# Performance work log

Measured on AMD Instinct MI355X. Metric: run time of the kernel, lower is better.

The kernel has to match this reference:

```python
import jax, jax.numpy as jnp
import numpy as np

B, IN, H = 1024, 2048, 2048
W_BIT = A_BIT = I_BIT = R_BIT = 8


def fake_quant(x, bits):
    # brevitas CommonQuant: signed, narrow-range, const scale 1.0 ->
    # int scale s = 1/(2^(b-1)-1); q = clip(round(x/s), -n, n); dq = q*s.
    n = 2.0 ** (bits - 1) - 1.0
    q = jnp.clip(x * n, -n, n)
    q = q + jax.lax.stop_gradient(jnp.round(q) - q)  # STE round
    return q / n


def setup_inputs() -> dict:
    key = jax.random.key(0)
    ks = jax.random.split(key, 7)
    std = 1.0 / np.sqrt(H)  # reset_parameters: uniform(-std, std)
    return {
        "x": jax.random.normal(ks[0], (B, IN), jnp.float32),
        "hx": jax.random.normal(ks[1], (B, H), jnp.float32),
        "cx": jax.random.normal(ks[2], (B, H), jnp.float32),
        "w_x2h": jax.random.uniform(ks[3], (4 * H, IN), jnp.float32, -std, std),
        "b_x2h": jax.random.uniform(ks[4], (4 * H,), jnp.float32, -std, std),
        "w_h2h": jax.random.uniform(ks[5], (4 * H, H), jnp.float32, -std, std),
        "b_h2h": jax.random.uniform(ks[6], (4 * H,), jnp.float32, -std, std),
    }


def reference(x, hx, cx, w_x2h, b_x2h, w_h2h, b_h2h):
    x_q = fake_quant(x, I_BIT)                      # input_quant
    wx_q = fake_quant(w_x2h, W_BIT)                 # CommonWeightQuant
    wh_q = fake_quant(w_h2h, W_BIT)
    gates = (jnp.einsum('bi,gi->bg', x_q, wx_q) + b_x2h
             + jnp.einsum('bh,gh->bg', hx, wh_q) + b_h2h)  # [B, 4H]
    f, i, g, o = jnp.split(gates, 4, axis=1)        # forget, input, cell, out
    f = fake_quant(jax.nn.sigmoid(f), A_BIT)
    i = fake_quant(jax.nn.sigmoid(i), A_BIT)
    g = fake_quant(jnp.tanh(g), A_BIT)
    o = fake_quant(jax.nn.sigmoid(o), A_BIT)
    c_new = f * cx + i * g
    h_new = o * fake_quant(jnp.tanh(c_new), A_BIT)
    c_out = fake_quant(c_new, R_BIT)                # recurrent_quant
    return (h_new, c_out)
```

## Files before the change

kernel.cpp:

```cpp
#include <hip/hip_runtime.h>
#include <stdint.h>
#include <math.h>

typedef __attribute__((ext_vector_type(4))) int i32x4;
typedef __attribute__((ext_vector_type(4))) float f32x4;

#define GLD16(gp, lp)                                                     \
  __builtin_amdgcn_global_load_lds(                                       \
      (__attribute__((address_space(1))) void*)(gp),                      \
      (__attribute__((address_space(3))) void*)(lp), 16, 0, 0)

__global__ void __launch_bounds__(256) k_prep_w(const float* __restrict__ wx,
                                                const float* __restrict__ wh,
                                                signed char* __restrict__ Wq) {
  int i = blockIdx.x * 256 + threadIdx.x;
  int e = i << 2;
  int g = e >> 12;
  int c = e & 4095;
  const float* src = (c < 2048) ? (wx + g * 2048 + c) : (wh + g * 2048 + (c - 2048));
  float4 v = *(const float4*)src;
  char4 o;
  o.x = (signed char)(int)rint(fmin(fmax((double)v.x * 127.0, -127.0), 127.0));
  o.y = (signed char)(int)rint(fmin(fmax((double)v.y * 127.0, -127.0), 127.0));
  o.z = (signed char)(int)rint(fmin(fmax((double)v.z * 127.0, -127.0), 127.0));
  o.w = (signed char)(int)rint(fmin(fmax((double)v.w * 127.0, -127.0), 127.0));
  *(char4*)(Wq + e) = o;
}

__global__ void __launch_bounds__(256) k_prep_a(const float* __restrict__ x,
                                                const float* __restrict__ hx,
                                                signed char* __restrict__ Aq) {
  int i = blockIdx.x * 256 + threadIdx.x;
  int e = i << 2;
  int b = e >> 11;
  int c = e & 2047;
  float4 xv = *(const float4*)(x + b * 2048 + c);
  float4 hv = *(const float4*)(hx + b * 2048 + c);
  float xa[4] = {xv.x, xv.y, xv.z, xv.w};
  float ha[4] = {hv.x, hv.y, hv.z, hv.w};
  char4 q4, s1, s2, s3, s4, s5;
  signed char* qp = (signed char*)&q4;
  signed char* p1 = (signed char*)&s1;
  signed char* p2 = (signed char*)&s2;
  signed char* p3 = (signed char*)&s3;
  signed char* p4 = (signed char*)&s4;
  signed char* p5 = (signed char*)&s5;
  #pragma unroll
  for (int j = 0; j < 4; ++j) {
    qp[j] = (signed char)(int)rint(fmin(fmax((double)xa[j] * 127.0, -127.0), 127.0));
    double r = (double)ha[j];
    double d1 = rint(r * 16.0);     r -= d1 * 0x1p-4;
    double d2 = rint(r * 0x1p11);   r -= d2 * 0x1p-11;
    double d3 = rint(r * 0x1p18);   r -= d3 * 0x1p-18;
    double d4 = rint(r * 0x1p25);   r -= d4 * 0x1p-25;
    double d5 = rint(r * 0x1p32);
    p1[j] = (signed char)(int)d1;
    p2[j] = (signed char)(int)d2;
    p3[j] = (signed char)(int)d3;
    p4[j] = (signed char)(int)d4;
    p5[j] = (signed char)(int)d5;
  }
  size_t base = (size_t)b * 12288;
  *(char4*)(Aq + base + 0 * 2048 + c) = s5;
  *(char4*)(Aq + base + 1 * 2048 + c) = s4;
  *(char4*)(Aq + base + 2 * 2048 + c) = s3;
  *(char4*)(Aq + base + 3 * 2048 + c) = s2;
  *(char4*)(Aq + base + 4 * 2048 + c) = s1;
  *(char4*)(Aq + base + 5 * 2048 + c) = q4;
}

__global__ void __launch_bounds__(256, 3) k_gemm_lstm(
    const signed char* __restrict__ Aq, const signed char* __restrict__ Wq,
    const float* __restrict__ bx, const float* __restrict__ bh,
    const float* __restrict__ cx, float* __restrict__ out) {
  __shared__ __align__(16) signed char smem[24576];
  signed char* As = smem;
  signed char* Bs = smem + 16384;

  const int t  = threadIdx.x;
  const int wv = t >> 6;
  const int ln = t & 63;
  const int wm = wv & 1;
  const int wn = wv >> 1;
  const int lr = ln & 15;
  const int q  = ln >> 4;

  const int j0 = blockIdx.x * 16;
  const int m0 = blockIdx.y * 128;

  int sA[4];
  #pragma unroll
  for (int is = 0; is < 4; ++is) {
    int s = is * 256 + t;
    int r = s >> 3;
    int c = s & 7;
    int cp = c ^ (r & 7);
    sA[is] = (m0 + r) * 12288 + cp * 16;
  }
  int sB[2];
  #pragma unroll
  for (int is = 0; is < 2; ++is) {
    int s = is * 256 + t;
    int r = s >> 3;
    int c = s & 7;
    int cp = c ^ (r & 7);
    int wrow = (r >> 4) * 2048 + j0 + (r & 15);
    sB[is] = wrow * 4096 + cp * 16;
  }

  int aoff[4], boff[2];
  const int swz = lr & 7;
  #pragma unroll
  for (int mf = 0; mf < 4; ++mf)
    aoff[mf] = (wm * 64 + mf * 16 + lr) * 128 + ((q ^ swz) * 16);
  #pragma unroll
  for (int nf = 0; nf < 2; ++nf)
    boff[nf] = (wn * 32 + nf * 16 + lr) * 128 + ((q ^ swz) * 16);

  i32x4 acc[4][2];
  f32x4 Hh[4][2], Hl[4][2];
  #pragma unroll
  for (int mf = 0; mf < 4; ++mf)
    #pragma unroll
    for (int nf = 0; nf < 2; ++nf)
      acc[mf][nf] = (i32x4){0, 0, 0, 0};

  #pragma unroll 1
  for (int ph = 0; ph < 6; ++ph) {
    const int kA = ph * 2048;
    const int kB = (ph < 5) ? 2048 : 0;
    #pragma unroll 1
    for (int it = 0; it < 16; ++it) {
      const int kk = it * 128;
      __syncthreads();
      #pragma unroll
      for (int is = 0; is < 4; ++is)
        GLD16(Aq + sA[is] + kA + kk, As + is * 4096 + wv * 1024);
      #pragma unroll
      for (int is = 0; is < 2; ++is)
        GLD16(Wq + sB[is] + kB + kk, Bs + is * 4096 + wv * 1024);
      asm volatile("s_waitcnt vmcnt(0)" ::: "memory");
      __syncthreads();
      #pragma unroll
      for (int s = 0; s < 2; ++s) {
        const int sx = s << 6;
        i32x4 af[4], bf[2];
        #pragma unroll
        for (int mf = 0; mf < 4; ++mf) af[mf] = *(const i32x4*)&As[aoff[mf] ^ sx];
        #pragma unroll
        for (int nf = 0; nf < 2; ++nf) bf[nf] = *(const i32x4*)&Bs[boff[nf] ^ sx];
        #pragma unroll
        for (int mf = 0; mf < 4; ++mf)
          #pragma unroll
          for (int nf = 0; nf < 2; ++nf)
            acc[mf][nf] = __builtin_amdgcn_mfma_i32_16x16x64_i8(
                af[mf], bf[nf], acc[mf][nf], 0, 0, 0);
      }
    }
    if (ph == 0) {
      #pragma unroll
      for (int mf = 0; mf < 4; ++mf)
        #pragma unroll
        for (int nf = 0; nf < 2; ++nf) {
          #pragma unroll
          for (int r = 0; r < 4; ++r) {
            Hh[mf][nf][r] = (float)acc[mf][nf][r];
            Hl[mf][nf][r] = 0.f;
          }
          acc[mf][nf] = (i32x4){0, 0, 0, 0};
        }
    } else if (ph < 5) {
      #pragma unroll
      for (int mf = 0; mf < 4; ++mf)
        #pragma unroll
        for (int nf = 0; nf < 2; ++nf) {
          #pragma unroll
          for (int r = 0; r < 4; ++r) {
            float tv = Hh[mf][nf][r] * 0x1p-7f;
            float S  = (float)acc[mf][nf][r];
            float sm = tv + S;
            float z  = sm - tv;
            float e  = (tv - (sm - z)) + (S - z);
            Hl[mf][nf][r] = Hl[mf][nf][r] * 0x1p-7f + e;
            Hh[mf][nf][r] = sm;
          }
          acc[mf][nf] = (i32x4){0, 0, 0, 0};
        }
    }
  }

  const double invsq = 1.0 / 16129.0;
  const double hsc   = 0x1p-4 / 127.0;

  float (*Lgo)[128][17] = (float(*)[128][17])smem;

  __syncthreads();
  if (wn == 1) {
    #pragma unroll
    for (int mf = 0; mf < 4; ++mf) {
      #pragma unroll
      for (int nf = 0; nf < 2; ++nf) {
        int gate = 2 + nf;
        int gcol = gate * 2048 + j0 + lr;
        double bsum = (double)bx[gcol] + (double)bh[gcol];
        #pragma unroll
        for (int r = 0; r < 4; ++r) {
          double Sx = (double)acc[mf][nf][r];
          double Hd = ((double)Hh[mf][nf][r] + (double)Hl[mf][nf][r]) * hsc;
          double pre = Sx * invsq + Hd + bsum;
          double av = (gate == 2) ? tanh(pre) : (1.0 / (1.0 + exp(-pre)));
          double qv = rint(fmin(fmax(av * 127.0, -127.0), 127.0));
          int m = wm * 64 + mf * 16 + q * 4 + r;
          Lgo[nf][m][lr] = (float)qv;
        }
      }
    }
  }
  __syncthreads();
  if (wn == 0) {
    #pragma unroll
    for (int mf = 0; mf < 4; ++mf) {
      int gcf = j0 + lr;
      int gci = 2048 + j0 + lr;
      double bf_ = (double)bx[gcf] + (double)bh[gcf];
      double bi_ = (double)bx[gci] + (double)bh[gci];
      #pragma unroll
      for (int r = 0; r < 4; ++r) {
        int m = wm * 64 + mf * 16 + q * 4 + r;
        double fpre = (double)acc[mf][0][r] * invsq +
                      ((double)Hh[mf][0][r] + (double)Hl[mf][0][r]) * hsc + bf_;
        double ipre = (double)acc[mf][1][r] * invsq +
                      ((double)Hh[mf][1][r] + (double)Hl[mf][1][r]) * hsc + bi_;
        double fs = 1.0 / (1.0 + exp(-fpre));
        double is = 1.0 / (1.0 + exp(-ipre));
        double fv = rint(fmin(fmax(fs * 127.0, -127.0), 127.0)) / 127.0;
        double iv = rint(fmin(fmax(is * 127.0, -127.0), 127.0)) / 127.0;
        double gv = (double)Lgo[0][m][lr] / 127.0;
        double ov = (double)Lgo[1][m][lr] / 127.0;
        int row = m0 + m;
        int col = j0 + lr;
        double cn = fv * (double)cx[row * 2048 + col] + iv * gv;
        double tq = rint(fmin(fmax(tanh(cn) * 127.0, -127.0), 127.0)) / 127.0;
        double hv = ov * tq;
        double cq = rint(fmin(fmax(cn * 127.0, -127.0), 127.0)) / 127.0;
        out[row * 2048 + col] = (float)hv;
        out[2097152 + row * 2048 + col] = (float)cq;
      }
    }
  }
}

extern "C" void kernel_launch(void* const* d_in, const int* in_sizes, int n_in,
                              void* d_out, int out_size, void* d_ws, size_t ws_size,
                              hipStream_t stream) {
  const float* x  = (const float*)d_in[0];
  const float* hx = (const float*)d_in[1];
  const float* cx = (const float*)d_in[2];
  const float* wx = (const float*)d_in[3];
  const float* bx = (const float*)d_in[4];
  const float* wh = (const float*)d_in[5];
  const float* bh = (const float*)d_in[6];
  float* out = (float*)d_out;

  signed char* Wq = (signed char*)d_ws;
  signed char* Aq = (signed char*)d_ws + 33554432;

  k_prep_w<<<dim3(32768), dim3(256), 0, stream>>>(wx, wh, Wq);
  k_prep_a<<<dim3(2048), dim3(256), 0, stream>>>(x, hx, Aq);
  k_gemm_lstm<<<dim3(128, 8), dim3(256), 0, stream>>>(Aq, Wq, bx, bh, cx, out);
}
```

Measured before the change: 389.3 us.

## Double-buffer LDS tiles to overlap global loads with MFMA compute

Flattens the phase/iteration loops into a single 96-step loop and uses two LDS buffers so the next K-tile is fetched with global_load_lds while the current tile feeds the int8 MFMAs. This drops one barrier per iteration and hides global-load latency behind compute. It doubles shared memory per block, which could limit occupancy.

```diff
diff --git a/kernel.cpp b/kernel.cpp
--- a/kernel.cpp
+++ b/kernel.cpp
@@ -73,9 +73,7 @@
     const signed char* __restrict__ Aq, const signed char* __restrict__ Wq,
     const float* __restrict__ bx, const float* __restrict__ bh,
     const float* __restrict__ cx, float* __restrict__ out) {
-  __shared__ __align__(16) signed char smem[24576];
-  signed char* As = smem;
-  signed char* Bs = smem + 16384;
+  __shared__ __align__(16) signed char smem[49152];
 
   const int t  = threadIdx.x;
   const int wv = t >> 6;
@@ -125,68 +123,90 @@
     for (int nf = 0; nf < 2; ++nf)
       acc[mf][nf] = (i32x4){0, 0, 0, 0};
 
+  {
+    #pragma unroll
+    for (int is = 0; is < 4; ++is)
+      GLD16(Aq + sA[is], smem + is * 4096 + wv * 1024);
+    #pragma unroll
+    for (int is = 0; is < 2; ++is)
+      GLD16(Wq + sB[is] + 2048, smem + 16384 + is * 4096 + wv * 1024);
+  }
+  asm volatile("s_waitcnt vmcnt(0)" ::: "memory");
+  __syncthreads();
+
+  int lbase = 0;
   #pragma unroll 1
-  for (int ph = 0; ph < 6; ++ph) {
-    const int kA = ph * 2048;
-    const int kB = (ph < 5) ? 2048 : 0;
-    #pragma unroll 1
-    for (int it = 0; it < 16; ++it) {
-      const int kk = it * 128;
-      __syncthreads();
+  for (int g = 0; g < 96; ++g) {
+    if (g < 95) {
+      const int gn  = g + 1;
+      const int phn = gn >> 4;
+      const int kkn = (gn & 15) << 7;
+      const int kAn = phn * 2048 + kkn;
+      const int kBn = ((phn < 5) ? 2048 : 0) + kkn;
+      const int nb  = lbase ^ 24576;
       #pragma unroll
       for (int is = 0; is < 4; ++is)
-        GLD16(Aq + sA[is] + kA + kk, As + is * 4096 + wv * 1024);
+        GLD16(Aq + sA[is] + kAn, smem + nb + is * 4096 + wv * 1024);
       #pragma unroll
       for (int is = 0; is < 2; ++is)
-        GLD16(Wq + sB[is] + kB + kk, Bs + is * 4096 + wv * 1024);
-      asm volatile("s_waitcnt vmcnt(0)" ::: "memory");
-      __syncthreads();
-      #pragma unroll
-      for (int s = 0; s < 2; ++s) {
-        const int sx = s << 6;
-        i32x4 af[4], bf[2];
-        #pragma unroll
-        for (int mf = 0; mf < 4; ++mf) af[mf] = *(const i32x4*)&As[aoff[mf] ^ sx];
-        #pragma unroll
-        for (int nf = 0; nf < 2; ++nf) bf[nf] = *(const i32x4*)&Bs[boff[nf] ^ sx];
+        GLD16(Wq + sB[is] + kBn, smem + nb + 16384 + is * 4096 + wv * 1024);
+    }
+
+    const signed char* As = smem + lbase;
+    const signed char* Bs = smem + lbase + 16384;
+    #pragma unroll
+    for (int s = 0; s < 2; ++s) {
+      const int sx = s << 6;
+      i32x4 af[4], bf[2];
+      #pragma unroll
+      for (int mf = 0; mf < 4; ++mf) af[mf] = *(const i32x4*)&As[aoff[mf] ^ sx];
+      #pragma unroll
+      for (int nf = 0; nf < 2; ++nf) bf[nf] = *(const i32x4*)&Bs[boff[nf] ^ sx];
+      #pragma unroll
+      for (int mf = 0; mf < 4; ++mf)
+        #pragma unroll
+        for (int nf = 0; nf < 2; ++nf)
+          acc[mf][nf] = __builtin_amdgcn_mfma_i32_16x16x64_i8(
+              af[mf], bf[nf], acc[mf][nf], 0, 0, 0);
+    }
+
+    if ((g & 15) == 15) {
+      const int ph = g >> 4;
+      if (ph == 0) {
         #pragma unroll
         for (int mf = 0; mf < 4; ++mf)
           #pragma unroll
-          for (int nf = 0; nf < 2; ++nf)
-            acc[mf][nf] = __builtin_amdgcn_mfma_i32_16x16x64_i8(
-                af[mf], bf[nf], acc[mf][nf], 0, 0, 0);
+          for (int nf = 0; nf < 2; ++nf) {
+            #pragma unroll
+            for (int r = 0; r < 4; ++r) {
+              Hh[mf][nf][r] = (float)acc[mf][nf][r];
+              Hl[mf][nf][r] = 0.f;
+            }
+            acc[mf][nf] = (i32x4){0, 0, 0, 0};
+          }
+      } else if (ph < 5) {
+        #pragma unroll
+        for (int mf = 0; mf < 4; ++mf)
+          #pragma unroll
+          for (int nf = 0; nf < 2; ++nf) {
+            #pragma unroll
+            for (int r = 0; r < 4; ++r) {
+              float tv = Hh[mf][nf][r] * 0x1p-7f;
+              float S  = (float)acc[mf][nf][r];
+              float sm = tv + S;
+              float z  = sm - tv;
+              float e  = (tv - (sm - z)) + (S - z);
+              Hl[mf][nf][r] = Hl[mf][nf][r] * 0x1p-7f + e;
+              Hh[mf][nf][r] = sm;
+            }
+            acc[mf][nf] = (i32x4){0, 0, 0, 0};
+          }
       }
     }
-    if (ph == 0) {
-      #pragma unroll
-      for (int mf = 0; mf < 4; ++mf)
-        #pragma unroll
-        for (int nf = 0; nf < 2; ++nf) {
-          #pragma unroll
-          for (int r = 0; r < 4; ++r) {
-            Hh[mf][nf][r] = (float)acc[mf][nf][r];
-            Hl[mf][nf][r] = 0.f;
-          }
-          acc[mf][nf] = (i32x4){0, 0, 0, 0};
-        }
-    } else if (ph < 5) {
-      #pragma unroll
-      for (int mf = 0; mf < 4; ++mf)
-        #pragma unroll
-        for (int nf = 0; nf < 2; ++nf) {
-          #pragma unroll
-          for (int r = 0; r < 4; ++r) {
-            float tv = Hh[mf][nf][r] * 0x1p-7f;
-            float S  = (float)acc[mf][nf][r];
-            float sm = tv + S;
-            float z  = sm - tv;
-            float e  = (tv - (sm - z)) + (S - z);
-            Hl[mf][nf][r] = Hl[mf][nf][r] * 0x1p-7f + e;
-            Hh[mf][nf][r] = sm;
-          }
-          acc[mf][nf] = (i32x4){0, 0, 0, 0};
-        }
-    }
+
+    asm volatile("s_waitcnt vmcnt(0)" ::: "memory");
+    __syncthreads();
+    lbase ^= 24576;
   }
 
   const double invsq = 1.0 / 16129.0;
@@ -194,7 +214,6 @@
 
   float (*Lgo)[128][17] = (float(*)[128][17])smem;
 
-  __syncthreads();
   if (wn == 1) {
     #pragma unroll
     for (int mf = 0; mf < 4; ++mf) {
```

Measured after the change: 360.8 us. 7.3% less time.

## Triple-buffer A tiles in LDS and stream W fragments directly into registers

Applied to the files above, without the earlier changes.

The K loop becomes one flat software-pipelined loop of 96 steps. A tiles are prefetched two steps ahead into three rotating LDS buffers using async global-to-LDS loads. W fragments skip LDS and are loaded straight into double-buffered registers one step ahead. Each step uses a single barrier with a partial vmcnt wait, and the per-phase accumulator folding moves into the loop body. The aim is to hide global-load latency behind the MFMA work and drop the double sync per iteration. In exchange, LDS use doubles to 48 KB and register pressure rises, which could limit occupancy under the 3-block launch bound.

```diff
diff --git a/kernel.cpp b/kernel.cpp
--- a/kernel.cpp
+++ b/kernel.cpp
@@ -73,9 +73,7 @@
     const signed char* __restrict__ Aq, const signed char* __restrict__ Wq,
     const float* __restrict__ bx, const float* __restrict__ bh,
     const float* __restrict__ cx, float* __restrict__ out) {
-  __shared__ __align__(16) signed char smem[24576];
-  signed char* As = smem;
-  signed char* Bs = smem + 16384;
+  __shared__ __align__(16) signed char smem[49152];
 
   const int t  = threadIdx.x;
   const int wv = t >> 6;
@@ -97,25 +95,17 @@
     int cp = c ^ (r & 7);
     sA[is] = (m0 + r) * 12288 + cp * 16;
   }
-  int sB[2];
-  #pragma unroll
-  for (int is = 0; is < 2; ++is) {
-    int s = is * 256 + t;
-    int r = s >> 3;
-    int c = s & 7;
-    int cp = c ^ (r & 7);
-    int wrow = (r >> 4) * 2048 + j0 + (r & 15);
-    sB[is] = wrow * 4096 + cp * 16;
-  }
-
-  int aoff[4], boff[2];
+
+  int aoff[4];
   const int swz = lr & 7;
   #pragma unroll
   for (int mf = 0; mf < 4; ++mf)
     aoff[mf] = (wm * 64 + mf * 16 + lr) * 128 + ((q ^ swz) * 16);
+
+  const signed char* pB[2];
   #pragma unroll
   for (int nf = 0; nf < 2; ++nf)
-    boff[nf] = (wn * 32 + nf * 16 + lr) * 128 + ((q ^ swz) * 16);
+    pB[nf] = Wq + (size_t)((wn * 2 + nf) * 2048 + j0 + lr) * 4096 + q * 16;
 
   i32x4 acc[4][2];
   f32x4 Hh[4][2], Hl[4][2];
@@ -125,69 +115,116 @@
     for (int nf = 0; nf < 2; ++nf)
       acc[mf][nf] = (i32x4){0, 0, 0, 0};
 
+  i32x4 B0[2][2], B1[2][2];
+
+  {
+    #pragma unroll
+    for (int is = 0; is < 4; ++is)
+      GLD16(Aq + sA[is], smem + is * 4096 + wv * 1024);
+    #pragma unroll
+    for (int is = 0; is < 4; ++is)
+      GLD16(Aq + sA[is] + 128, smem + 16384 + is * 4096 + wv * 1024);
+    #pragma unroll
+    for (int nf = 0; nf < 2; ++nf)
+      #pragma unroll
+      for (int s = 0; s < 2; ++s)
+        B0[nf][s] = *(const i32x4*)(pB[nf] + 2048 + s * 64);
+  }
+  asm volatile("s_waitcnt vmcnt(0)" ::: "memory");
+  __builtin_amdgcn_s_barrier();
+  __builtin_amdgcn_sched_barrier(0);
+
+  int cur = 0;
+  int stg = 32768;
+
+#define FOLD(G)                                                            \
+  if (((G) & 15) == 15) {                                                  \
+    const int ph_ = (G) >> 4;                                              \
+    if (ph_ == 0) {                                                        \
+      _Pragma("unroll")                                                    \
+      for (int mf = 0; mf < 4; ++mf)                                       \
+        _Pragma("unroll")                                                  \
+        for (int nf = 0; nf < 2; ++nf) {                                   \
+          _Pragma("unroll")                                                \
+          for (int r = 0; r < 4; ++r) {                                    \
+            Hh[mf][nf][r] = (float)acc[mf][nf][r];                         \
+            Hl[mf][nf][r] = 0.f;                                           \
+          }                                                                \
+          acc[mf][nf] = (i32x4){0, 0, 0, 0};                               \
+        }                                                                  \
+    } else if (ph_ < 5) {                                                  \
+      _Pragma("unroll")                                                    \
+      for (int mf = 0; mf < 4; ++mf)                                       \
+        _Pragma("unroll")                                                  \
+        for (int nf = 0; nf < 2; ++nf) {                                   \
+          _Pragma("unroll")                                                \
+          for (int r = 0; r < 4; ++r) {                                    \
+            float tv = Hh[mf][nf][r] * 0x1p-7f;          \
+            float S  = (float)acc[mf][nf][r];        \
+            float sm = tv + S;                                             \
+            float z  = sm - tv;                                            \
+            float e  = (tv - (sm - z)) + (S - z);                          \
+            Hl[mf][nf][r] = Hl[mf][nf][r] * 0x1p-7f + e;                   \
+            Hh[mf][nf][r] = sm;                                            \
+          }                                                                \
+          acc[mf][nf] = (i32x4){0, 0, 0, 0};                               \
+        }                                                                  \
+    }                                                                      \
+  }
+
+#define KBODY(G, BC, BN, DO_STAGE, DO_BLOAD, VMC) do {                     \
+    if (DO_STAGE) {                                      \
+      const int gn_  = (G) + 2;                                            \
+      const int kAn_ = (gn_ >> 4) * 2048 + ((gn_ & 15) << 7);              \
+      _Pragma("unroll")                                                    \
+      for (int is = 0; is < 4; ++is)                                       \
+        GLD16(Aq + sA[is] + kAn_, smem + stg + is * 4096 + wv * 1024);     \
+    }                                                                      \
+    __builtin_amdgcn_sched_barrier(0);                                     \
+    {                          \
+      const signed char* As_ = smem + cur;                                 \
+      _Pragma("unroll")                                                    \
+      for (int s = 0; s < 2; ++s) {                                        \
+        const int sx_ = s << 6;                                            \
+        i32x4 af_[4];                                                      \
+        _Pragma("unroll")                                                  \
+        for (int mf = 0; mf < 4; ++mf)                                     \
+          af_[mf] = *(const i32x4*)&As_[aoff[mf] ^ sx_];                   \
+        _Pragma("unroll")                                                  \
+        for (int mf = 0; mf < 4; ++mf)                                     \
+          _Pragma("unroll")                                                \
+          for (int nf = 0; nf < 2; ++nf)                                   \
+            acc[mf][nf] = __builtin_amdgcn_mfma_i32_16x16x64_i8(           \
+                af_[mf], (BC)[nf][s], acc[mf][nf], 0, 0, 0);               \
+      }                                                                    \
+    }                                                                      \
+    if (DO_BLOAD) {              \
+      const int gb_  = (G) + 1;                                            \
+      const int kBn_ = (((gb_ >> 4) < 5) ? 2048 : 0) + ((gb_ & 15) << 7);  \
+      _Pragma("unroll")                                                    \
+      for (int nf = 0; nf < 2; ++nf)                                       \
+        _Pragma("unroll")                                                  \
+        for (int s = 0; s < 2; ++s)                                        \
+          (BN)[nf][s] = *(const i32x4*)(pB[nf] + kBn_ + s * 64);           \
+    }                                                                      \
+    FOLD(G);                                                               \
+    __builtin_amdgcn_sched_barrier(0);                                     \
+    asm volatile("s_waitcnt vmcnt(" #VMC ")" ::: "memory");                \
+    __builtin_amdgcn_s_barrier();         \
+    __builtin_amdgcn_sched_barrier(0);                                     \
+    cur += 16384; if (cur == 49152) cur = 0;                               \
+    stg += 16384; if (stg == 49152) stg = 0;                               \
+  } while (0)
+
   #pragma unroll 1
-  for (int ph = 0; ph < 6; ++ph) {
-    const int kA = ph * 2048;
-    const int kB = (ph < 5) ? 2048 : 0;
-    #pragma unroll 1
-    for (int it = 0; it < 16; ++it) {
-      const int kk = it * 128;
-      __syncthreads();
-      #pragma unroll
-      for (int is = 0; is < 4; ++is)
-        GLD16(Aq + sA[is] + kA + kk, As + is * 4096 + wv * 1024);
-      #pragma unroll
-      for (int is = 0; is < 2; ++is)
-        GLD16(Wq + sB[is] + kB + kk, Bs + is * 4096 + wv * 1024);
-      asm volatile("s_waitcnt vmcnt(0)" ::: "memory");
-      __syncthreads();
-      #pragma unroll
-      for (int s = 0; s < 2; ++s) {
-        const int sx = s << 6;
-        i32x4 af[4], bf[2];
-        #pragma unroll
-        for (int mf = 0; mf < 4; ++mf) af[mf] = *(const i32x4*)&As[aoff[mf] ^ sx];
-        #pragma unroll
-        for (int nf = 0; nf < 2; ++nf) bf[nf] = *(const i32x4*)&Bs[boff[nf] ^ sx];
-        #pragma unroll
-        for (int mf = 0; mf < 4; ++mf)
-          #pragma unroll
-          for (int nf = 0; nf < 2; ++nf)
-            acc[mf][nf] = __builtin_amdgcn_mfma_i32_16x16x64_i8(
-                af[mf], bf[nf], acc[mf][nf], 0, 0, 0);
-      }
-    }
-    if (ph == 0) {
-      #pragma unroll
-      for (int mf = 0; mf < 4; ++mf)
-        #pragma unroll
-        for (int nf = 0; nf < 2; ++nf) {
-          #pragma unroll
-          for (int r = 0; r < 4; ++r) {
-            Hh[mf][nf][r] = (float)acc[mf][nf][r];
-            Hl[mf][nf][r] = 0.f;
-          }
-          acc[mf][nf] = (i32x4){0, 0, 0, 0};
-        }
-    } else if (ph < 5) {
-      #pragma unroll
-      for (int mf = 0; mf < 4; ++mf)
-        #pragma unroll
-        for (int nf = 0; nf < 2; ++nf) {
-          #pragma unroll
-          for (int r = 0; r < 4; ++r) {
-            float tv = Hh[mf][nf][r] * 0x1p-7f;
-            float S  = (float)acc[mf][nf][r];
-            float sm = tv + S;
-            float z  = sm - tv;
-            float e  = (tv - (sm - z)) + (S - z);
-            Hl[mf][nf][r] = Hl[mf][nf][r] * 0x1p-7f + e;
-            Hh[mf][nf][r] = sm;
-          }
-          acc[mf][nf] = (i32x4){0, 0, 0, 0};
-        }
-    }
-  }
+  for (int g = 0; g < 94; g += 2) {
+    KBODY(g,     B0, B1, 1, 1, 8);
+    KBODY(g + 1, B1, B0, 1, 1, 8);
+  }
+  KBODY(94, B0, B1, 0, 1, 8);
+  KBODY(95, B1, B0, 0, 0, 0);
+#undef KBODY
+#undef FOLD
 
   const double invsq = 1.0 / 16129.0;
   const double hsc   = 0x1p-4 / 127.0;
```

New measurement: 456.3 us. 17.2% more time.
